# Kernel tuning notes

Hardware: AMD Instinct MI355X
Metric: run time of the kernel (lower is better)

## Reference

```python
import jax, jax.numpy as jnp
import numpy as np

N_NODES = 50000

def spmm(rows, cols, vals, x):
    # sparse [n,n] @ dense [n,d] via gather + segment_sum
    gathered = vals[:, None] * x[cols]          # [E, d]
    return jax.ops.segment_sum(gathered, rows, num_segments=N_NODES)

def setup_inputs() -> dict:
    key = jax.random.key(0)
    k1, k2, k3, k4, k5, k6 = jax.random.split(key, 6)
    embeddings = jax.random.normal(k1, (N_NODES, 128), dtype=jnp.float32)
    adj_rows = jax.random.randint(k2, (800000,), 0, N_NODES, dtype=jnp.int32)
    adj_cols = jax.random.randint(k3, (800000,), 0, N_NODES, dtype=jnp.int32)
    adj_vals = jax.random.uniform(k4, (800000,), dtype=jnp.float32)
    W1 = jax.random.normal(k5, (128, 128), dtype=jnp.float32) * 0.05
    W2 = jax.random.normal(k6, (128, 64), dtype=jnp.float32) * 0.05
    return {"embeddings": embeddings, "adj_rows": adj_rows, "adj_cols": adj_cols,
            "adj_vals": adj_vals, "W1": W1, "W2": W2}

def reference(embeddings, adj_rows, adj_cols, adj_vals, W1, W2):
    # layer 1: SpMM -> dense GEMM -> ReLU
    h = jax.nn.relu(spmm(adj_rows, adj_cols, adj_vals, embeddings) @ W1)
    # layer 2: SpMM -> dense GEMM (no nonlinearity)
    logits = spmm(adj_rows, adj_cols, adj_vals, h) @ W2
    return jax.nn.softmax(logits, axis=1)
```

## Files before the change

### kernel.cpp

```cpp
#include <hip/hip_runtime.h>
#include <cmath>

#define N_NODES 50000
#define DIM 128
#define DOUT 64
#define SCAN_NB 196

typedef float f32x4 __attribute__((ext_vector_type(4)));
typedef short bf16x8 __attribute__((ext_vector_type(8)));
typedef float f32x4v __attribute__((ext_vector_type(4)));

__device__ __forceinline__ unsigned short f2bf(float f) {
  unsigned int u = __float_as_uint(f);
  u = (u + 0x7fffu + ((u >> 16) & 1u)) >> 16;
  return (unsigned short)u;
}
__device__ __forceinline__ float bf2f(unsigned short h) {
  return __uint_as_float((unsigned int)h << 16);
}
__device__ __forceinline__ float bflo(unsigned int q) {
  return __uint_as_float(q << 16);
}
__device__ __forceinline__ float bfhi(unsigned int q) {
  return __uint_as_float(q & 0xffff0000u);
}


__global__ __launch_bounds__(256) void off_kernel(
    const int* __restrict__ rows, int* __restrict__ deg,
    int* __restrict__ localoff, int E) {
  int e = blockIdx.x * blockDim.x + threadIdx.x;
  if (e < E) localoff[e] = atomicAdd(&deg[rows[e]], 1);
}

__global__ __launch_bounds__(256) void scan_blk_kernel(
    const int* __restrict__ deg, int* __restrict__ incl,
    int* __restrict__ partials) {
  __shared__ int s[256];
  int i = blockIdx.x * 256 + threadIdx.x;
  int v = (i < N_NODES) ? deg[i] : 0;
  s[threadIdx.x] = v;
  __syncthreads();
  for (int o = 1; o < 256; o <<= 1) {
    int t = (threadIdx.x >= (unsigned)o) ? s[threadIdx.x - o] : 0;
    __syncthreads();
    s[threadIdx.x] += t;
    __syncthreads();
  }
  if (i < N_NODES) incl[i] = s[threadIdx.x];
  if (threadIdx.x == 255) partials[blockIdx.x] = s[255];
}

__global__ __launch_bounds__(256) void scan_part_kernel(
    int* __restrict__ partials, int* __restrict__ rowptr, int E) {
  __shared__ int s[256];
  int v = (threadIdx.x < SCAN_NB) ? partials[threadIdx.x] : 0;
  s[threadIdx.x] = v;
  __syncthreads();
  for (int o = 1; o < 256; o <<= 1) {
    int t = (threadIdx.x >= (unsigned)o) ? s[threadIdx.x - o] : 0;
    __syncthreads();
    s[threadIdx.x] += t;
    __syncthreads();
  }
  if (threadIdx.x < SCAN_NB) partials[threadIdx.x] = s[threadIdx.x] - v;
  if (threadIdx.x == 0) rowptr[N_NODES] = E;
}

__global__ __launch_bounds__(256) void scan_add_kernel(
    const int* __restrict__ incl, const int* __restrict__ deg,
    const int* __restrict__ partials, int* __restrict__ rowptr) {
  int i = blockIdx.x * 256 + threadIdx.x;
  if (i < N_NODES)
    rowptr[i] = incl[i] - deg[i] + partials[blockIdx.x];
}

__global__ __launch_bounds__(256) void scatter_kernel(
    const int* __restrict__ rows, const int* __restrict__ cols,
    const float* __restrict__ vals, const int* __restrict__ rowptr,
    const int* __restrict__ localoff, int2* __restrict__ edges, int E) {
  int e = blockIdx.x * blockDim.x + threadIdx.x;
  if (e < E) {
    int p = rowptr[rows[e]] + localoff[e];
    edges[p] = make_int2(cols[e], __float_as_int(vals[e]));
  }
}

__global__ __launch_bounds__(256) void wtrans_kernel(
    const float* __restrict__ W1, const float* __restrict__ W2,
    unsigned short* __restrict__ W1th, unsigned short* __restrict__ W1tl,
    unsigned short* __restrict__ W2th, unsigned short* __restrict__ W2tl) {
  int i = blockIdx.x * 256 + threadIdx.x;
  if (i < 128 * 128) {
    int c = i >> 7, k = i & 127;
    float v = W1[k * 128 + c];
    unsigned short h = f2bf(v);
    W1th[i] = h;
    W1tl[i] = f2bf(v - bf2f(h));
  } else if (i < 128 * 128 + 64 * 128) {
    int j = i - 128 * 128;
    int c = j >> 7, k = j & 127;
    float v = W2[k * 64 + c];
    unsigned short h = f2bf(v);
    W2th[j] = h;
    W2tl[j] = f2bf(v - bf2f(h));
  }
}

template <int N, bool XSPLIT>
__global__ __launch_bounds__(256) void gemm_mfma_kernel(
    const void* __restrict__ xin,
    const unsigned short* __restrict__ Wth,
    const unsigned short* __restrict__ Wtl,
    unsigned short* __restrict__ y,
    int M) {
  __shared__ unsigned short sXh[64 * 136];
  __shared__ unsigned short sXl[XSPLIT ? 64 * 136 : 1];
  __shared__ unsigned short sWh[64 * 136];
  __shared__ unsigned short sWl[64 * 136];
  const int cb = blockIdx.y;
  const int row0 = blockIdx.x * 64;
  const int tid = threadIdx.x;

  if constexpr (XSPLIT) {
    const float* x = (const float*)xin;
    for (int i = tid; i < 64 * 16; i += 256) {
      int r = i >> 4, g = i & 15;
      int gr = row0 + r; if (gr >= M) gr = M - 1;
      const f32x4* src = reinterpret_cast<const f32x4*>(x + (size_t)gr * 128 + g * 8);
      f32x4 a = src[0], b = src[1];
      unsigned short* dh = &sXh[r * 136 + g * 8];
      unsigned short* dl = &sXl[r * 136 + g * 8];
      float v[8] = {a.x, a.y, a.z, a.w, b.x, b.y, b.z, b.w};
#pragma unroll
      for (int j = 0; j < 8; ++j) {
        unsigned short h = f2bf(v[j]);
        dh[j] = h;
        dl[j] = f2bf(v[j] - bf2f(h));
      }
    }
  } else {
    const uint4* xq = (const uint4*)xin;
    for (int i = tid; i < 64 * 16; i += 256) {
      int r = i >> 4, g = i & 15;
      int gr = row0 + r; if (gr >= M) gr = M - 1;
      *reinterpret_cast<uint4*>(&sXh[r * 136 + g * 8]) = xq[(size_t)gr * 16 + g];
    }
  }
  {
    const uint4* wh = (const uint4*)Wth;
    const uint4* wl = (const uint4*)Wtl;
    for (int i = tid; i < 64 * 16; i += 256) {
      int c = i >> 4, g = i & 15;
      size_t src = (size_t)(cb * 64 + c) * 16 + g;
      *reinterpret_cast<uint4*>(&sWh[c * 136 + g * 8]) = wh[src];
      *reinterpret_cast<uint4*>(&sWl[c * 136 + g * 8]) = wl[src];
    }
  }
  __syncthreads();

  const int lane = tid & 63;
  const int w = tid >> 6;
  const int r = lane & 15;
  const int q = lane >> 4;

  bf16x8 ah[4], al[4];
#pragma unroll
  for (int k = 0; k < 4; ++k) {
    ah[k] = *reinterpret_cast<const bf16x8*>(&sXh[(w * 16 + r) * 136 + k * 32 + q * 8]);
    if constexpr (XSPLIT)
      al[k] = *reinterpret_cast<const bf16x8*>(&sXl[(w * 16 + r) * 136 + k * 32 + q * 8]);
  }

  f32x4v acc[4] = {{0.f,0.f,0.f,0.f},{0.f,0.f,0.f,0.f},{0.f,0.f,0.f,0.f},{0.f,0.f,0.f,0.f}};
#pragma unroll
  for (int k = 0; k < 4; ++k) {
#pragma unroll
    for (int n = 0; n < 4; ++n) {
      bf16x8 bh = *reinterpret_cast<const bf16x8*>(&sWh[(n * 16 + r) * 136 + k * 32 + q * 8]);
      bf16x8 bl = *reinterpret_cast<const bf16x8*>(&sWl[(n * 16 + r) * 136 + k * 32 + q * 8]);
      acc[n] = __builtin_amdgcn_mfma_f32_16x16x32_bf16(ah[k], bh, acc[n], 0, 0, 0);
      acc[n] = __builtin_amdgcn_mfma_f32_16x16x32_bf16(ah[k], bl, acc[n], 0, 0, 0);
      if constexpr (XSPLIT)
        acc[n] = __builtin_amdgcn_mfma_f32_16x16x32_bf16(al[k], bh, acc[n], 0, 0, 0);
    }
  }

#pragma unroll
  for (int n = 0; n < 4; ++n) {
#pragma unroll
    for (int j = 0; j < 4; ++j) {
      int gr = row0 + w * 16 + q * 4 + j;
      if (gr < M)
        y[(size_t)gr * N + cb * 64 + n * 16 + r] = f2bf(acc[n][j]);
    }
  }
}

__global__ __launch_bounds__(256) void spmm_relu_kernel(
    const int* __restrict__ rowptr, const int2* __restrict__ edges,
    const unsigned int* __restrict__ t1q,
    unsigned int* __restrict__ hq) {
  const int row = blockIdx.x * 4 + (threadIdx.x >> 6);
  const int lane = threadIdx.x & 63;
  const int beg = rowptr[row];
  const int end = rowptr[row + 1];
  float ax = 0.f, ay = 0.f;
  int i = beg;
  for (; i + 8 <= end; i += 8) {
    int2 e0 = edges[i],     e1 = edges[i + 1], e2 = edges[i + 2], e3 = edges[i + 3];
    int2 e4 = edges[i + 4], e5 = edges[i + 5], e6 = edges[i + 6], e7 = edges[i + 7];
    unsigned int q0 = t1q[(size_t)e0.x * 64 + lane];
    unsigned int q1 = t1q[(size_t)e1.x * 64 + lane];
    unsigned int q2 = t1q[(size_t)e2.x * 64 + lane];
    unsigned int q3 = t1q[(size_t)e3.x * 64 + lane];
    unsigned int q4 = t1q[(size_t)e4.x * 64 + lane];
    unsigned int q5 = t1q[(size_t)e5.x * 64 + lane];
    unsigned int q6 = t1q[(size_t)e6.x * 64 + lane];
    unsigned int q7 = t1q[(size_t)e7.x * 64 + lane];
    float w0 = __int_as_float(e0.y), w1 = __int_as_float(e1.y);
    float w2 = __int_as_float(e2.y), w3 = __int_as_float(e3.y);
    float w4 = __int_as_float(e4.y), w5 = __int_as_float(e5.y);
    float w6 = __int_as_float(e6.y), w7 = __int_as_float(e7.y);
    ax += w0 * bflo(q0) + w1 * bflo(q1) + w2 * bflo(q2) + w3 * bflo(q3) +
          w4 * bflo(q4) + w5 * bflo(q5) + w6 * bflo(q6) + w7 * bflo(q7);
    ay += w0 * bfhi(q0) + w1 * bfhi(q1) + w2 * bfhi(q2) + w3 * bfhi(q3) +
          w4 * bfhi(q4) + w5 * bfhi(q5) + w6 * bfhi(q6) + w7 * bfhi(q7);
  }
  for (; i + 2 <= end; i += 2) {
    int2 e0 = edges[i], e1 = edges[i + 1];
    unsigned int q0 = t1q[(size_t)e0.x * 64 + lane];
    unsigned int q1 = t1q[(size_t)e1.x * 64 + lane];
    float w0 = __int_as_float(e0.y), w1 = __int_as_float(e1.y);
    ax += w0 * bflo(q0) + w1 * bflo(q1);
    ay += w0 * bfhi(q0) + w1 * bfhi(q1);
  }
  if (i < end) {
    int2 e = edges[i];
    unsigned int q = t1q[(size_t)e.x * 64 + lane];
    float w = __int_as_float(e.y);
    ax += w * bflo(q);
    ay += w * bfhi(q);
  }
  ax = fmaxf(ax, 0.f);
  ay = fmaxf(ay, 0.f);
  hq[(size_t)row * 64 + lane] =
      (unsigned int)f2bf(ax) | ((unsigned int)f2bf(ay) << 16);
}

__global__ __launch_bounds__(256) void spmm_softmax_kernel(
    const int* __restrict__ rowptr, const int2* __restrict__ edges,
    const unsigned int* __restrict__ t2q,
    float* __restrict__ out) {
  const int row = blockIdx.x * 4 + (threadIdx.x >> 6);
  const int lane = threadIdx.x & 63;
  const int sub = lane >> 5;
  const int sl = lane & 31;
  const int beg = rowptr[row];
  const int end = rowptr[row + 1];
  float ax = 0.f, ay = 0.f;
  int i = beg;
  for (; i + 8 <= end; i += 8) {
    int2 ea = edges[i + sub];
    int2 eb = edges[i + 2 + sub];
    int2 ec = edges[i + 4 + sub];
    int2 ed = edges[i + 6 + sub];
    unsigned int qa = t2q[(size_t)ea.x * 32 + sl];
    unsigned int qb = t2q[(size_t)eb.x * 32 + sl];
    unsigned int qc = t2q[(size_t)ec.x * 32 + sl];
    unsigned int qd = t2q[(size_t)ed.x * 32 + sl];
    float va = __int_as_float(ea.y), vb = __int_as_float(eb.y);
    float vc = __int_as_float(ec.y), vd = __int_as_float(ed.y);
    ax += va * bflo(qa) + vb * bflo(qb) + vc * bflo(qc) + vd * bflo(qd);
    ay += va * bfhi(qa) + vb * bfhi(qb) + vc * bfhi(qc) + vd * bfhi(qd);
  }
  for (; i < end; i += 2) {
    int j = i + sub;
    bool ok = j < end;
    int2 e = edges[ok ? j : end - 1];
    float v = ok ? __int_as_float(e.y) : 0.f;
    unsigned int q = t2q[(size_t)e.x * 32 + sl];
    ax += v * bflo(q);
    ay += v * bfhi(q);
  }
  ax += __shfl_xor(ax, 32);
  ay += __shfl_xor(ay, 32);
  float m = fmaxf(ax, ay);
  for (int o = 16; o >= 1; o >>= 1) m = fmaxf(m, __shfl_xor(m, o));
  float ex = expf(ax - m), ey = expf(ay - m);
  float s = ex + ey;
  for (int o = 16; o >= 1; o >>= 1) s += __shfl_xor(s, o);
  if (sub == 0)
    reinterpret_cast<float2*>(out)[(size_t)row * 32 + sl] =
        make_float2(ex / s, ey / s);
}

extern "C" void kernel_launch(void* const* d_in, const int* in_sizes, int n_in,
                              void* d_out, int out_size, void* d_ws, size_t ws_size,
                              hipStream_t stream) {
  const float* emb   = (const float*)d_in[0];
  const int*   arows = (const int*)d_in[1];
  const int*   acols = (const int*)d_in[2];
  const float* avals = (const float*)d_in[3];
  const float* W1    = (const float*)d_in[4];
  const float* W2    = (const float*)d_in[5];
  float* out = (float*)d_out;
  const int E = in_sizes[1];

  const size_t hbytes = (size_t)N_NODES * DIM * sizeof(float);
  char* p = (char*)d_ws;
  char*  bufA   = p;         p += hbytes;
  char*  bufB   = p;         p += hbytes;
  int2*  edges  = (int2*)p;  p += (size_t)E * sizeof(int2);
  int*   deg    = (int*)p;   p += (size_t)N_NODES * sizeof(int);
  int*   rowptr = (int*)p;   p += (size_t)(N_NODES + 1) * sizeof(int);
  unsigned short* W1th = (unsigned short*)p; p += 128 * 128 * 2;
  unsigned short* W1tl = (unsigned short*)p; p += 128 * 128 * 2;
  unsigned short* W2th = (unsigned short*)p; p += 64 * 128 * 2;
  unsigned short* W2tl = (unsigned short*)p; p += 64 * 128 * 2;
  int* incl     = (int*)edges;
  int* partials = ((int*)edges) + N_NODES;
  int* localoff = (int*)bufB;

  hipMemsetAsync(deg, 0, (size_t)N_NODES * sizeof(int), stream);

  const int eblocks = (E + 255) / 256;

  wtrans_kernel<<<96, 256, 0, stream>>>(W1, W2, W1th, W1tl, W2th, W2tl);

  off_kernel<<<eblocks, 256, 0, stream>>>(arows, deg, localoff, E);
  scan_blk_kernel<<<SCAN_NB, 256, 0, stream>>>(deg, incl, partials);
  scan_part_kernel<<<1, 256, 0, stream>>>(partials, rowptr, E);
  scan_add_kernel<<<SCAN_NB, 256, 0, stream>>>(incl, deg, partials, rowptr);
  scatter_kernel<<<eblocks, 256, 0, stream>>>(arows, acols, avals, rowptr,
                                              localoff, edges, E);

  const int gblocks = (N_NODES + 63) / 64;

  gemm_mfma_kernel<128, true><<<dim3(gblocks, 2), 256, 0, stream>>>(
      emb, W1th, W1tl, (unsigned short*)bufA, N_NODES);
  spmm_relu_kernel<<<N_NODES / 4, 256, 0, stream>>>(
      rowptr, edges, (const unsigned int*)bufA, (unsigned int*)bufB);
  gemm_mfma_kernel<64, false><<<dim3(gblocks, 1), 256, 0, stream>>>(
      bufB, W2th, W2tl, (unsigned short*)bufA, N_NODES);
  spmm_softmax_kernel<<<N_NODES / 4, 256, 0, stream>>>(
      rowptr, edges, (const unsigned int*)bufA, out);
}
```

Before: 232.7 us.

## Fuse all stages into one persistent cooperative kernel with grid syncs

Replaces the chain of eleven separate launches (memset, weight transpose, degree count, three-stage scan, scatter, two GEMMs, two SpMMs) with a single cooperative persistent kernel whose phases are separated by grid-wide barriers. The GEMMs become per-wave 16-row tiles that read weights directly from global memory instead of staging them in LDS, and the first GEMM covers all 128 output columns per tile. The scan's second pass is folded into a per-block reduction over the preceding partials. This is meant to remove launch gaps and tail effects, at the cost of grid.sync overhead, a grid capped at 1024 blocks, and GEMMs that lose LDS reuse of the weights.

Result: slower. 845.5 us (+263.4%).

```diff
diff --git a/kernel.cpp b/kernel.cpp
--- a/kernel.cpp
+++ b/kernel.cpp
@@ -1,14 +1,15 @@
 #include <hip/hip_runtime.h>
+#include <hip/hip_cooperative_groups.h>
 #include <cmath>
 
+namespace cg = cooperative_groups;
+
 #define N_NODES 50000
-#define DIM 128
-#define DOUT 64
 #define SCAN_NB 196
+#define NTILES  3125
 
 typedef float f32x4 __attribute__((ext_vector_type(4)));
 typedef short bf16x8 __attribute__((ext_vector_type(8)));
-typedef float f32x4v __attribute__((ext_vector_type(4)));
 
 __device__ __forceinline__ unsigned short f2bf(float f) {
   unsigned int u = __float_as_uint(f);
@@ -25,274 +26,262 @@
   return __uint_as_float(q & 0xffff0000u);
 }
 
-
-__global__ __launch_bounds__(256) void off_kernel(
-    const int* __restrict__ rows, int* __restrict__ deg,
-    int* __restrict__ localoff, int E) {
-  int e = blockIdx.x * blockDim.x + threadIdx.x;
-  if (e < E) localoff[e] = atomicAdd(&deg[rows[e]], 1);
-}
-
-__global__ __launch_bounds__(256) void scan_blk_kernel(
-    const int* __restrict__ deg, int* __restrict__ incl,
-    int* __restrict__ partials) {
+__global__ __launch_bounds__(256, 4) void mega_kernel(
+    const float* __restrict__ emb, const int* __restrict__ arows,
+    const int* __restrict__ acols, const float* __restrict__ avals,
+    const float* __restrict__ W1, const float* __restrict__ W2,
+    float* __restrict__ out,
+    unsigned short* __restrict__ t1,
+    unsigned int* __restrict__ hq,
+    int2* __restrict__ edges, int* __restrict__ deg, int* __restrict__ rowptr,
+    int* __restrict__ partials,
+    unsigned short* __restrict__ W1th, unsigned short* __restrict__ W1tl,
+    unsigned short* __restrict__ W2th, unsigned short* __restrict__ W2tl,
+    int* __restrict__ localoff, int* __restrict__ incl,
+    int E) {
+  cg::grid_group grid = cg::this_grid();
   __shared__ int s[256];
-  int i = blockIdx.x * 256 + threadIdx.x;
-  int v = (i < N_NODES) ? deg[i] : 0;
-  s[threadIdx.x] = v;
-  __syncthreads();
-  for (int o = 1; o < 256; o <<= 1) {
-    int t = (threadIdx.x >= (unsigned)o) ? s[threadIdx.x - o] : 0;
-    __syncthreads();
-    s[threadIdx.x] += t;
-    __syncthreads();
-  }
-  if (i < N_NODES) incl[i] = s[threadIdx.x];
-  if (threadIdx.x == 255) partials[blockIdx.x] = s[255];
-}
-
-__global__ __launch_bounds__(256) void scan_part_kernel(
-    int* __restrict__ partials, int* __restrict__ rowptr, int E) {
-  __shared__ int s[256];
-  int v = (threadIdx.x < SCAN_NB) ? partials[threadIdx.x] : 0;
-  s[threadIdx.x] = v;
-  __syncthreads();
-  for (int o = 1; o < 256; o <<= 1) {
-    int t = (threadIdx.x >= (unsigned)o) ? s[threadIdx.x - o] : 0;
-    __syncthreads();
-    s[threadIdx.x] += t;
-    __syncthreads();
-  }
-  if (threadIdx.x < SCAN_NB) partials[threadIdx.x] = s[threadIdx.x] - v;
-  if (threadIdx.x == 0) rowptr[N_NODES] = E;
-}
-
-__global__ __launch_bounds__(256) void scan_add_kernel(
-    const int* __restrict__ incl, const int* __restrict__ deg,
-    const int* __restrict__ partials, int* __restrict__ rowptr) {
-  int i = blockIdx.x * 256 + threadIdx.x;
-  if (i < N_NODES)
-    rowptr[i] = incl[i] - deg[i] + partials[blockIdx.x];
-}
-
-__global__ __launch_bounds__(256) void scatter_kernel(
-    const int* __restrict__ rows, const int* __restrict__ cols,
-    const float* __restrict__ vals, const int* __restrict__ rowptr,
-    const int* __restrict__ localoff, int2* __restrict__ edges, int E) {
-  int e = blockIdx.x * blockDim.x + threadIdx.x;
-  if (e < E) {
-    int p = rowptr[rows[e]] + localoff[e];
-    edges[p] = make_int2(cols[e], __float_as_int(vals[e]));
-  }
-}
-
-__global__ __launch_bounds__(256) void wtrans_kernel(
-    const float* __restrict__ W1, const float* __restrict__ W2,
-    unsigned short* __restrict__ W1th, unsigned short* __restrict__ W1tl,
-    unsigned short* __restrict__ W2th, unsigned short* __restrict__ W2tl) {
-  int i = blockIdx.x * 256 + threadIdx.x;
-  if (i < 128 * 128) {
+  const int tid = threadIdx.x;
+  const int gtid = blockIdx.x * 256 + tid;
+  const int gsz = gridDim.x * 256;
+  const int lane = tid & 63;
+  const int wid = (blockIdx.x << 2) | (tid >> 6);
+  const int nwaves = gridDim.x << 2;
+
+  for (int i = gtid; i < N_NODES; i += gsz) deg[i] = 0;
+  for (int i = gtid; i < 128 * 128; i += gsz) {
     int c = i >> 7, k = i & 127;
     float v = W1[k * 128 + c];
     unsigned short h = f2bf(v);
     W1th[i] = h;
     W1tl[i] = f2bf(v - bf2f(h));
-  } else if (i < 128 * 128 + 64 * 128) {
-    int j = i - 128 * 128;
-    int c = j >> 7, k = j & 127;
+  }
+  for (int i = gtid; i < 64 * 128; i += gsz) {
+    int c = i >> 7, k = i & 127;
     float v = W2[k * 64 + c];
     unsigned short h = f2bf(v);
-    W2th[j] = h;
-    W2tl[j] = f2bf(v - bf2f(h));
-  }
-}
-
-template <int N, bool XSPLIT>
-__global__ __launch_bounds__(256) void gemm_mfma_kernel(
-    const void* __restrict__ xin,
-    const unsigned short* __restrict__ Wth,
-    const unsigned short* __restrict__ Wtl,
-    unsigned short* __restrict__ y,
-    int M) {
-  __shared__ unsigned short sXh[64 * 136];
-  __shared__ unsigned short sXl[XSPLIT ? 64 * 136 : 1];
-  __shared__ unsigned short sWh[64 * 136];
-  __shared__ unsigned short sWl[64 * 136];
-  const int cb = blockIdx.y;
-  const int row0 = blockIdx.x * 64;
-  const int tid = threadIdx.x;
-
-  if constexpr (XSPLIT) {
-    const float* x = (const float*)xin;
-    for (int i = tid; i < 64 * 16; i += 256) {
-      int r = i >> 4, g = i & 15;
-      int gr = row0 + r; if (gr >= M) gr = M - 1;
-      const f32x4* src = reinterpret_cast<const f32x4*>(x + (size_t)gr * 128 + g * 8);
-      f32x4 a = src[0], b = src[1];
-      unsigned short* dh = &sXh[r * 136 + g * 8];
-      unsigned short* dl = &sXl[r * 136 + g * 8];
-      float v[8] = {a.x, a.y, a.z, a.w, b.x, b.y, b.z, b.w};
-#pragma unroll
-      for (int j = 0; j < 8; ++j) {
-        unsigned short h = f2bf(v[j]);
-        dh[j] = h;
-        dl[j] = f2bf(v[j] - bf2f(h));
-      }
-    }
-  } else {
-    const uint4* xq = (const uint4*)xin;
-    for (int i = tid; i < 64 * 16; i += 256) {
-      int r = i >> 4, g = i & 15;
-      int gr = row0 + r; if (gr >= M) gr = M - 1;
-      *reinterpret_cast<uint4*>(&sXh[r * 136 + g * 8]) = xq[(size_t)gr * 16 + g];
-    }
-  }
+    W2th[i] = h;
+    W2tl[i] = f2bf(v - bf2f(h));
+  }
+  grid.sync();
+
+  for (int e = gtid; e < E; e += gsz)
+    localoff[e] = atomicAdd(&deg[arows[e]], 1);
+  grid.sync();
+
+  if (blockIdx.x < SCAN_NB) {
+    int i = blockIdx.x * 256 + tid;
+    int v = (i < N_NODES) ? deg[i] : 0;
+    s[tid] = v;
+    __syncthreads();
+    for (int o = 1; o < 256; o <<= 1) {
+      int t = (tid >= o) ? s[tid - o] : 0;
+      __syncthreads();
+      s[tid] += t;
+      __syncthreads();
+    }
+    if (i < N_NODES) incl[i] = s[tid];
+    if (tid == 255) partials[blockIdx.x] = s[255];
+  }
+  grid.sync();
+
+  if (blockIdx.x < SCAN_NB) {
+    s[tid] = (tid < (int)blockIdx.x) ? partials[tid] : 0;
+    __syncthreads();
+    for (int o = 128; o >= 1; o >>= 1) {
+      if (tid < o) s[tid] += s[tid + o];
+      __syncthreads();
+    }
+    int off = s[0];
+    int i = blockIdx.x * 256 + tid;
+    if (i < N_NODES) rowptr[i] = incl[i] - deg[i] + off;
+  }
+  if (gtid == 0) rowptr[N_NODES] = E;
+  grid.sync();
+
+  for (int e = gtid; e < E; e += gsz) {
+    int p = rowptr[arows[e]] + localoff[e];
+    edges[p] = make_int2(acols[e], __float_as_int(avals[e]));
+  }
+  grid.sync();
+
   {
-    const uint4* wh = (const uint4*)Wth;
-    const uint4* wl = (const uint4*)Wtl;
-    for (int i = tid; i < 64 * 16; i += 256) {
-      int c = i >> 4, g = i & 15;
-      size_t src = (size_t)(cb * 64 + c) * 16 + g;
-      *reinterpret_cast<uint4*>(&sWh[c * 136 + g * 8]) = wh[src];
-      *reinterpret_cast<uint4*>(&sWl[c * 136 + g * 8]) = wl[src];
-    }
-  }
-  __syncthreads();
-
-  const int lane = tid & 63;
-  const int w = tid >> 6;
-  const int r = lane & 15;
-  const int q = lane >> 4;
-
-  bf16x8 ah[4], al[4];
-#pragma unroll
-  for (int k = 0; k < 4; ++k) {
-    ah[k] = *reinterpret_cast<const bf16x8*>(&sXh[(w * 16 + r) * 136 + k * 32 + q * 8]);
-    if constexpr (XSPLIT)
-      al[k] = *reinterpret_cast<const bf16x8*>(&sXl[(w * 16 + r) * 136 + k * 32 + q * 8]);
-  }
-
-  f32x4v acc[4] = {{0.f,0.f,0.f,0.f},{0.f,0.f,0.f,0.f},{0.f,0.f,0.f,0.f},{0.f,0.f,0.f,0.f}};
-#pragma unroll
-  for (int k = 0; k < 4; ++k) {
-#pragma unroll
-    for (int n = 0; n < 4; ++n) {
-      bf16x8 bh = *reinterpret_cast<const bf16x8*>(&sWh[(n * 16 + r) * 136 + k * 32 + q * 8]);
-      bf16x8 bl = *reinterpret_cast<const bf16x8*>(&sWl[(n * 16 + r) * 136 + k * 32 + q * 8]);
-      acc[n] = __builtin_amdgcn_mfma_f32_16x16x32_bf16(ah[k], bh, acc[n], 0, 0, 0);
-      acc[n] = __builtin_amdgcn_mfma_f32_16x16x32_bf16(ah[k], bl, acc[n], 0, 0, 0);
-      if constexpr (XSPLIT)
-        acc[n] = __builtin_amdgcn_mfma_f32_16x16x32_bf16(al[k], bh, acc[n], 0, 0, 0);
-    }
-  }
-
-#pragma unroll
-  for (int n = 0; n < 4; ++n) {
-#pragma unroll
-    for (int j = 0; j < 4; ++j) {
-      int gr = row0 + w * 16 + q * 4 + j;
-      if (gr < M)
-        y[(size_t)gr * N + cb * 64 + n * 16 + r] = f2bf(acc[n][j]);
-    }
-  }
-}
-
-__global__ __launch_bounds__(256) void spmm_relu_kernel(
-    const int* __restrict__ rowptr, const int2* __restrict__ edges,
-    const unsigned int* __restrict__ t1q,
-    unsigned int* __restrict__ hq) {
-  const int row = blockIdx.x * 4 + (threadIdx.x >> 6);
-  const int lane = threadIdx.x & 63;
-  const int beg = rowptr[row];
-  const int end = rowptr[row + 1];
-  float ax = 0.f, ay = 0.f;
-  int i = beg;
-  for (; i + 8 <= end; i += 8) {
-    int2 e0 = edges[i],     e1 = edges[i + 1], e2 = edges[i + 2], e3 = edges[i + 3];
-    int2 e4 = edges[i + 4], e5 = edges[i + 5], e6 = edges[i + 6], e7 = edges[i + 7];
-    unsigned int q0 = t1q[(size_t)e0.x * 64 + lane];
-    unsigned int q1 = t1q[(size_t)e1.x * 64 + lane];
-    unsigned int q2 = t1q[(size_t)e2.x * 64 + lane];
-    unsigned int q3 = t1q[(size_t)e3.x * 64 + lane];
-    unsigned int q4 = t1q[(size_t)e4.x * 64 + lane];
-    unsigned int q5 = t1q[(size_t)e5.x * 64 + lane];
-    unsigned int q6 = t1q[(size_t)e6.x * 64 + lane];
-    unsigned int q7 = t1q[(size_t)e7.x * 64 + lane];
-    float w0 = __int_as_float(e0.y), w1 = __int_as_float(e1.y);
-    float w2 = __int_as_float(e2.y), w3 = __int_as_float(e3.y);
-    float w4 = __int_as_float(e4.y), w5 = __int_as_float(e5.y);
-    float w6 = __int_as_float(e6.y), w7 = __int_as_float(e7.y);
-    ax += w0 * bflo(q0) + w1 * bflo(q1) + w2 * bflo(q2) + w3 * bflo(q3) +
-          w4 * bflo(q4) + w5 * bflo(q5) + w6 * bflo(q6) + w7 * bflo(q7);
-    ay += w0 * bfhi(q0) + w1 * bfhi(q1) + w2 * bfhi(q2) + w3 * bfhi(q3) +
-          w4 * bfhi(q4) + w5 * bfhi(q5) + w6 * bfhi(q6) + w7 * bfhi(q7);
-  }
-  for (; i + 2 <= end; i += 2) {
-    int2 e0 = edges[i], e1 = edges[i + 1];
-    unsigned int q0 = t1q[(size_t)e0.x * 64 + lane];
-    unsigned int q1 = t1q[(size_t)e1.x * 64 + lane];
-    float w0 = __int_as_float(e0.y), w1 = __int_as_float(e1.y);
-    ax += w0 * bflo(q0) + w1 * bflo(q1);
-    ay += w0 * bfhi(q0) + w1 * bfhi(q1);
-  }
-  if (i < end) {
-    int2 e = edges[i];
-    unsigned int q = t1q[(size_t)e.x * 64 + lane];
-    float w = __int_as_float(e.y);
-    ax += w * bflo(q);
-    ay += w * bfhi(q);
-  }
-  ax = fmaxf(ax, 0.f);
-  ay = fmaxf(ay, 0.f);
-  hq[(size_t)row * 64 + lane] =
-      (unsigned int)f2bf(ax) | ((unsigned int)f2bf(ay) << 16);
-}
-
-__global__ __launch_bounds__(256) void spmm_softmax_kernel(
-    const int* __restrict__ rowptr, const int2* __restrict__ edges,
-    const unsigned int* __restrict__ t2q,
-    float* __restrict__ out) {
-  const int row = blockIdx.x * 4 + (threadIdx.x >> 6);
-  const int lane = threadIdx.x & 63;
-  const int sub = lane >> 5;
-  const int sl = lane & 31;
-  const int beg = rowptr[row];
-  const int end = rowptr[row + 1];
-  float ax = 0.f, ay = 0.f;
-  int i = beg;
-  for (; i + 8 <= end; i += 8) {
-    int2 ea = edges[i + sub];
-    int2 eb = edges[i + 2 + sub];
-    int2 ec = edges[i + 4 + sub];
-    int2 ed = edges[i + 6 + sub];
-    unsigned int qa = t2q[(size_t)ea.x * 32 + sl];
-    unsigned int qb = t2q[(size_t)eb.x * 32 + sl];
-    unsigned int qc = t2q[(size_t)ec.x * 32 + sl];
-    unsigned int qd = t2q[(size_t)ed.x * 32 + sl];
-    float va = __int_as_float(ea.y), vb = __int_as_float(eb.y);
-    float vc = __int_as_float(ec.y), vd = __int_as_float(ed.y);
-    ax += va * bflo(qa) + vb * bflo(qb) + vc * bflo(qc) + vd * bflo(qd);
-    ay += va * bfhi(qa) + vb * bfhi(qb) + vc * bfhi(qc) + vd * bfhi(qd);
-  }
-  for (; i < end; i += 2) {
-    int j = i + sub;
-    bool ok = j < end;
-    int2 e = edges[ok ? j : end - 1];
-    float v = ok ? __int_as_float(e.y) : 0.f;
-    unsigned int q = t2q[(size_t)e.x * 32 + sl];
-    ax += v * bflo(q);
-    ay += v * bfhi(q);
-  }
-  ax += __shfl_xor(ax, 32);
-  ay += __shfl_xor(ay, 32);
-  float m = fmaxf(ax, ay);
-  for (int o = 16; o >= 1; o >>= 1) m = fmaxf(m, __shfl_xor(m, o));
-  float ex = expf(ax - m), ey = expf(ay - m);
-  float s = ex + ey;
-  for (int o = 16; o >= 1; o >>= 1) s += __shfl_xor(s, o);
-  if (sub == 0)
-    reinterpret_cast<float2*>(out)[(size_t)row * 32 + sl] =
-        make_float2(ex / s, ey / s);
+    const int r = lane & 15, q = lane >> 4;
+    for (int t = wid; t < NTILES; t += nwaves) {
+      const float* xr = emb + (size_t)(t * 16 + r) * 128;
+      bf16x8 ah[4], al[4];
+#pragma unroll
+      for (int k = 0; k < 4; ++k) {
+        const f32x4* src = reinterpret_cast<const f32x4*>(xr + k * 32 + q * 8);
+        f32x4 a0 = src[0], a1 = src[1];
+        bf16x8 h8, l8;
+#pragma unroll
+        for (int j = 0; j < 4; ++j) {
+          unsigned short h = f2bf(a0[j]);
+          h8[j] = (short)h;
+          l8[j] = (short)f2bf(a0[j] - bf2f(h));
+        }
+#pragma unroll
+        for (int j = 0; j < 4; ++j) {
+          unsigned short h = f2bf(a1[j]);
+          h8[4 + j] = (short)h;
+          l8[4 + j] = (short)f2bf(a1[j] - bf2f(h));
+        }
+        ah[k] = h8;
+        al[k] = l8;
+      }
+      f32x4 acc[8];
+#pragma unroll
+      for (int n = 0; n < 8; ++n) acc[n] = (f32x4){0.f, 0.f, 0.f, 0.f};
+#pragma unroll
+      for (int k = 0; k < 4; ++k) {
+#pragma unroll
+        for (int n = 0; n < 8; ++n) {
+          bf16x8 bh = *reinterpret_cast<const bf16x8*>(
+              &W1th[(size_t)(n * 16 + r) * 128 + k * 32 + q * 8]);
+          bf16x8 bl = *reinterpret_cast<const bf16x8*>(
+              &W1tl[(size_t)(n * 16 + r) * 128 + k * 32 + q * 8]);
+          acc[n] = __builtin_amdgcn_mfma_f32_16x16x32_bf16(ah[k], bh, acc[n], 0, 0, 0);
+          acc[n] = __builtin_amdgcn_mfma_f32_16x16x32_bf16(ah[k], bl, acc[n], 0, 0, 0);
+          acc[n] = __builtin_amdgcn_mfma_f32_16x16x32_bf16(al[k], bh, acc[n], 0, 0, 0);
+        }
+      }
+#pragma unroll
+      for (int n = 0; n < 8; ++n)
+#pragma unroll
+        for (int j = 0; j < 4; ++j)
+          t1[(size_t)(t * 16 + q * 4 + j) * 128 + n * 16 + r] = f2bf(acc[n][j]);
+    }
+  }
+  grid.sync();
+
+  {
+    const unsigned int* t1q = (const unsigned int*)t1;
+    for (int row = wid; row < N_NODES; row += nwaves) {
+      const int beg = rowptr[row];
+      const int end = rowptr[row + 1];
+      float ax = 0.f, ay = 0.f;
+      int i = beg;
+      for (; i + 8 <= end; i += 8) {
+        int2 e0 = edges[i],     e1 = edges[i + 1], e2 = edges[i + 2], e3 = edges[i + 3];
+        int2 e4 = edges[i + 4], e5 = edges[i + 5], e6 = edges[i + 6], e7 = edges[i + 7];
+        unsigned int q0 = t1q[(size_t)e0.x * 64 + lane];
+        unsigned int q1 = t1q[(size_t)e1.x * 64 + lane];
+        unsigned int q2 = t1q[(size_t)e2.x * 64 + lane];
+        unsigned int q3 = t1q[(size_t)e3.x * 64 + lane];
+        unsigned int q4 = t1q[(size_t)e4.x * 64 + lane];
+        unsigned int q5 = t1q[(size_t)e5.x * 64 + lane];
+        unsigned int q6 = t1q[(size_t)e6.x * 64 + lane];
+        unsigned int q7 = t1q[(size_t)e7.x * 64 + lane];
+        float w0 = __int_as_float(e0.y), w1 = __int_as_float(e1.y);
+        float w2 = __int_as_float(e2.y), w3 = __int_as_float(e3.y);
+        float w4 = __int_as_float(e4.y), w5 = __int_as_float(e5.y);
+        float w6 = __int_as_float(e6.y), w7 = __int_as_float(e7.y);
+        ax += w0 * bflo(q0) + w1 * bflo(q1) + w2 * bflo(q2) + w3 * bflo(q3) +
+              w4 * bflo(q4) + w5 * bflo(q5) + w6 * bflo(q6) + w7 * bflo(q7);
+        ay += w0 * bfhi(q0) + w1 * bfhi(q1) + w2 * bfhi(q2) + w3 * bfhi(q3) +
+              w4 * bfhi(q4) + w5 * bfhi(q5) + w6 * bfhi(q6) + w7 * bfhi(q7);
+      }
+      for (; i + 2 <= end; i += 2) {
+        int2 e0 = edges[i], e1 = edges[i + 1];
+        unsigned int q0 = t1q[(size_t)e0.x * 64 + lane];
+        unsigned int q1 = t1q[(size_t)e1.x * 64 + lane];
+        float w0 = __int_as_float(e0.y), w1 = __int_as_float(e1.y);
+        ax += w0 * bflo(q0) + w1 * bflo(q1);
+        ay += w0 * bfhi(q0) + w1 * bfhi(q1);
+      }
+      if (i < end) {
+        int2 e = edges[i];
+        unsigned int q = t1q[(size_t)e.x * 64 + lane];
+        float w = __int_as_float(e.y);
+        ax += w * bflo(q);
+        ay += w * bfhi(q);
+      }
+      ax = fmaxf(ax, 0.f);
+      ay = fmaxf(ay, 0.f);
+      hq[(size_t)row * 64 + lane] =
+          (unsigned int)f2bf(ax) | ((unsigned int)f2bf(ay) << 16);
+    }
+  }
+  grid.sync();
+
+  {
+    unsigned short* t2 = t1;
+    const int r = lane & 15, q = lane >> 4;
+    for (int t = wid; t < NTILES; t += nwaves) {
+      const unsigned int* hr = hq + (size_t)(t * 16 + r) * 64;
+      bf16x8 a[4];
+#pragma unroll
+      for (int k = 0; k < 4; ++k)
+        a[k] = *reinterpret_cast<const bf16x8*>(hr + k * 16 + q * 4);
+      f32x4 acc[4];
+#pragma unroll
+      for (int n = 0; n < 4; ++n) acc[n] = (f32x4){0.f, 0.f, 0.f, 0.f};
+#pragma unroll
+      for (int k = 0; k < 4; ++k) {
+#pragma unroll
+        for (int n = 0; n < 4; ++n) {
+          bf16x8 bh = *reinterpret_cast<const bf16x8*>(
+              &W2th[(size_t)(n * 16 + r) * 128 + k * 32 + q * 8]);
+          bf16x8 bl = *reinterpret_cast<const bf16x8*>(
+              &W2tl[(size_t)(n * 16 + r) * 128 + k * 32 + q * 8]);
+          acc[n] = __builtin_amdgcn_mfma_f32_16x16x32_bf16(a[k], bh, acc[n], 0, 0, 0);
+          acc[n] = __builtin_amdgcn_mfma_f32_16x16x32_bf16(a[k], bl, acc[n], 0, 0, 0);
+        }
+      }
+#pragma unroll
+      for (int n = 0; n < 4; ++n)
+#pragma unroll
+        for (int j = 0; j < 4; ++j)
+          t2[(size_t)(t * 16 + q * 4 + j) * 64 + n * 16 + r] = f2bf(acc[n][j]);
+    }
+  }
+  grid.sync();
+
+  {
+    const unsigned int* t2q = (const unsigned int*)t1;
+    const int sub = lane >> 5;
+    const int sl = lane & 31;
+    for (int row = wid; row < N_NODES; row += nwaves) {
+      const int beg = rowptr[row];
+      const int end = rowptr[row + 1];
+      float ax = 0.f, ay = 0.f;
+      int i = beg;
+      for (; i + 8 <= end; i += 8) {
+        int2 ea = edges[i + sub];
+        int2 eb = edges[i + 2 + sub];
+        int2 ec = edges[i + 4 + sub];
+        int2 ed = edges[i + 6 + sub];
+        unsigned int qa = t2q[(size_t)ea.x * 32 + sl];
+        unsigned int qb = t2q[(size_t)eb.x * 32 + sl];
+        unsigned int qc = t2q[(size_t)ec.x * 32 + sl];
+        unsigned int qd = t2q[(size_t)ed.x * 32 + sl];
+        float va = __int_as_float(ea.y), vb = __int_as_float(eb.y);
+        float vc = __int_as_float(ec.y), vd = __int_as_float(ed.y);
+        ax += va * bflo(qa) + vb * bflo(qb) + vc * bflo(qc) + vd * bflo(qd);
+        ay += va * bfhi(qa) + vb * bfhi(qb) + vc * bfhi(qc) + vd * bfhi(qd);
+      }
+      for (; i < end; i += 2) {
+        int j = i + sub;
+        bool ok = j < end;
+        int2 e = edges[ok ? j : end - 1];
+        float v = ok ? __int_as_float(e.y) : 0.f;
+        unsigned int q = t2q[(size_t)e.x * 32 + sl];
+        ax += v * bflo(q);
+        ay += v * bfhi(q);
+      }
+      ax += __shfl_xor(ax, 32);
+      ay += __shfl_xor(ay, 32);
+      float m = fmaxf(ax, ay);
+      for (int o = 16; o >= 1; o >>= 1) m = fmaxf(m, __shfl_xor(m, o));
+      float ex = expf(ax - m), ey = expf(ay - m);
+      float ssum = ex + ey;
+      for (int o = 16; o >= 1; o >>= 1) ssum += __shfl_xor(ssum, o);
+      if (sub == 0)
+        reinterpret_cast<float2*>(out)[(size_t)row * 32 + sl] =
+            make_float2(ex / ssum, ey / ssum);
+    }
+  }
 }
 
 extern "C" void kernel_launch(void* const* d_in, const int* in_sizes, int n_in,
@@ -305,44 +294,35 @@
   const float* W1    = (const float*)d_in[4];
   const float* W2    = (const float*)d_in[5];
   float* out = (float*)d_out;
-  const int E = in_sizes[1];
-
-  const size_t hbytes = (size_t)N_NODES * DIM * sizeof(float);
+  int E = in_sizes[1];
+
+  const size_t hbytes = (size_t)N_NODES * 128 * sizeof(float);
   char* p = (char*)d_ws;
-  char*  bufA   = p;         p += hbytes;
-  char*  bufB   = p;         p += hbytes;
-  int2*  edges  = (int2*)p;  p += (size_t)E * sizeof(int2);
-  int*   deg    = (int*)p;   p += (size_t)N_NODES * sizeof(int);
-  int*   rowptr = (int*)p;   p += (size_t)(N_NODES + 1) * sizeof(int);
+  unsigned short* t1 = (unsigned short*)p; p += hbytes;
+  unsigned int*   hq = (unsigned int*)p;   p += hbytes;
+  int2* edges  = (int2*)p; p += (size_t)E * sizeof(int2);
+  int*  deg    = (int*)p;  p += (size_t)N_NODES * sizeof(int);
+  int*  rowptr = (int*)p;  p += (size_t)(N_NODES + 1) * sizeof(int);
+  int*  partials = (int*)p; p += 256 * sizeof(int);
   unsigned short* W1th = (unsigned short*)p; p += 128 * 128 * 2;
   unsigned short* W1tl = (unsigned short*)p; p += 128 * 128 * 2;
   unsigned short* W2th = (unsigned short*)p; p += 64 * 128 * 2;
   unsigned short* W2tl = (unsigned short*)p; p += 64 * 128 * 2;
   int* incl     = (int*)edges;
-  int* partials = ((int*)edges) + N_NODES;
-  int* localoff = (int*)bufB;
-
-  hipMemsetAsync(deg, 0, (size_t)N_NODES * sizeof(int), stream);
-
-  const int eblocks = (E + 255) / 256;
-
-  wtrans_kernel<<<96, 256, 0, stream>>>(W1, W2, W1th, W1tl, W2th, W2tl);
-
-  off_kernel<<<eblocks, 256, 0, stream>>>(arows, deg, localoff, E);
-  scan_blk_kernel<<<SCAN_NB, 256, 0, stream>>>(deg, incl, partials);
-  scan_part_kernel<<<1, 256, 0, stream>>>(partials, rowptr, E);
-  scan_add_kernel<<<SCAN_NB, 256, 0, stream>>>(incl, deg, partials, rowptr);
-  scatter_kernel<<<eblocks, 256, 0, stream>>>(arows, acols, avals, rowptr,
-                                              localoff, edges, E);
-
-  const int gblocks = (N_NODES + 63) / 64;
-
-  gemm_mfma_kernel<128, true><<<dim3(gblocks, 2), 256, 0, stream>>>(
-      emb, W1th, W1tl, (unsigned short*)bufA, N_NODES);
-  spmm_relu_kernel<<<N_NODES / 4, 256, 0, stream>>>(
-      rowptr, edges, (const unsigned int*)bufA, (unsigned int*)bufB);
-  gemm_mfma_kernel<64, false><<<dim3(gblocks, 1), 256, 0, stream>>>(
-      bufB, W2th, W2tl, (unsigned short*)bufA, N_NODES);
-  spmm_softmax_kernel<<<N_NODES / 4, 256, 0, stream>>>(
-      rowptr, edges, (const unsigned int*)bufA, out);
-}
+  int* localoff = (int*)hq;
+
+  int maxb = 4;
+  hipOccupancyMaxActiveBlocksPerMultiprocessor(&maxb, mega_kernel, 256, 0);
+  int nb = maxb * 256;
+  if (nb > 1024) nb = 1024;
+  if (nb < 256) nb = 256;
+
+  void* args[] = {(void*)&emb, (void*)&arows, (void*)&acols, (void*)&avals,
+                  (void*)&W1, (void*)&W2, (void*)&out,
+                  (void*)&t1, (void*)&hq, (void*)&edges, (void*)&deg,
+                  (void*)&rowptr, (void*)&partials,
+                  (void*)&W1th, (void*)&W1tl, (void*)&W2th, (void*)&W2tl,
+                  (void*)&localoff, (void*)&incl, (void*)&E};
+  hipLaunchCooperativeKernel((const void*)mega_kernel, dim3(nb), dim3(256),
+                             args, 0, stream);
+}
```
